# Kernel tuning notes

Hardware: AMD Instinct MI355X
Metric: run time of the kernel (lower is better)

Reference implementation:

```python
import jax, jax.numpy as jnp
import numpy as np

EPS = 1e-5

def _layer_norm(x, w, b):
    mu = jnp.mean(x, axis=-1, keepdims=True)
    var = jnp.mean(jnp.square(x - mu), axis=-1, keepdims=True)
    return (x - mu) * jax.lax.rsqrt(var + EPS) * w + b

def setup_inputs() -> dict:
    key = jax.random.key(0)
    ks = jax.random.split(key, 8)
    B, S, D = 8, 2048, 1024
    image_features = jax.random.normal(ks[0], (B, S, D), dtype=jnp.float32)
    text_features = jax.random.normal(ks[1], (B, S, D), dtype=jnp.float32)
    ln_w = jnp.ones((D,), dtype=jnp.float32)
    ln_b = jnp.zeros((D,), dtype=jnp.float32)
    lim = 1.0 / np.sqrt(D)
    W_img = jax.random.uniform(ks[2], (D, D), minval=-lim, maxval=lim, dtype=jnp.float32)
    b_img = jax.random.uniform(ks[3], (D,), minval=-lim, maxval=lim, dtype=jnp.float32)
    W_txt = jax.random.uniform(ks[4], (D, D), minval=-lim, maxval=lim, dtype=jnp.float32)
    b_txt = jax.random.uniform(ks[5], (D,), minval=-lim, maxval=lim, dtype=jnp.float32)
    return {"image_features": image_features, "text_features": text_features,
            "ln_w": ln_w, "ln_b": ln_b, "W_img": W_img, "b_img": b_img,
            "W_txt": W_txt, "b_txt": b_txt}

def reference(image_features, text_features, ln_w, ln_b, W_img, b_img, W_txt, b_txt):
    D = image_features.shape[-1]
    scale = D ** (-0.5)
    image_norm = _layer_norm(image_features, ln_w, ln_b)
    text_norm = _layer_norm(text_features, ln_w, ln_b)
    # torch Linear: x @ W^T + b
    image_proj = jnp.einsum('bsd,ed->bse', image_norm, W_img) + b_img  # [B,Si,D]
    text_proj = jnp.einsum('btd,ed->bte', text_norm, W_txt) + b_txt    # [B,St,D]
    attn = jnp.einsum('bsd,btd->bst', image_proj, text_proj) * scale   # [B,Si,St]
    attn = jax.nn.softmax(attn, axis=-1)
    image_out = jnp.einsum('bst,btd->bsd', attn, text_proj)            # [B,Si,D]
    text_out = jnp.einsum('bst,bsd->btd', attn, image_proj)            # [B,St,D]
    return (image_out, text_out)
```

## Files before the change

kernel.cpp:

```cpp
#include <hip/hip_runtime.h>


#define DEV __device__ __forceinline__

typedef short s16x8 __attribute__((ext_vector_type(8)));
typedef float f32x4 __attribute__((ext_vector_type(4)));

DEV unsigned short f2bf(float f){
  unsigned u = __float_as_uint(f);
  u = (u + 0x7fffu + ((u >> 16) & 1u)) >> 16;
  return (unsigned short)u;
}
DEV float bf2f(unsigned short s){ return __uint_as_float(((unsigned)s) << 16); }

DEV void ldsload16(const void* g, void* l){
  __builtin_amdgcn_global_load_lds((const __attribute__((address_space(1))) void*)g,
                                   (__attribute__((address_space(3))) void*)l, 16, 0, 0);
}

__global__ __launch_bounds__(256) void k_cvt2(const float* __restrict__ sa,
                                              const float* __restrict__ sb,
                                              unsigned short* __restrict__ da,
                                              unsigned short* __restrict__ db, int n4){
  int i = blockIdx.x * 256 + threadIdx.x;
  const float* s; unsigned short* d; int j;
  if (i < n4){ s = sa; d = da; j = i; }
  else       { s = sb; d = db; j = i - n4; if (j >= n4) return; }
  float4 v = ((const float4*)s)[j];
  ushort4 o;
  o.x = f2bf(v.x); o.y = f2bf(v.y); o.z = f2bf(v.z); o.w = f2bf(v.w);
  ((ushort4*)d)[j] = o;
}

__global__ __launch_bounds__(256) void k_ln2(const float* __restrict__ xa,
                                             const float* __restrict__ xb,
                                             const float* __restrict__ w,
                                             const float* __restrict__ b,
                                             unsigned short* __restrict__ ya,
                                             unsigned short* __restrict__ yb){
  int rb = blockIdx.x, tid = threadIdx.x;
  const float* x; unsigned short* y;
  if (rb < 16384){ x = xa; y = ya; } else { x = xb; y = yb; rb -= 16384; }
  float4 v = ((const float4*)(x + (size_t)rb * 1024))[tid];
  float s  = v.x + v.y + v.z + v.w;
  float s2 = v.x*v.x + v.y*v.y + v.z*v.z + v.w*v.w;
  #pragma unroll
  for (int o = 32; o > 0; o >>= 1){ s += __shfl_xor(s, o, 64); s2 += __shfl_xor(s2, o, 64); }
  __shared__ float sh[8];
  int wv = tid >> 6, ln = tid & 63;
  if (!ln){ sh[wv] = s; sh[4 + wv] = s2; }
  __syncthreads();
  s  = sh[0] + sh[1] + sh[2] + sh[3];
  s2 = sh[4] + sh[5] + sh[6] + sh[7];
  float mean = s * (1.f/1024.f);
  float var  = s2 * (1.f/1024.f) - mean * mean;
  float rstd = rsqrtf(var + 1e-5f);
  float4 w4 = ((const float4*)w)[tid];
  float4 b4 = ((const float4*)b)[tid];
  ushort4 o;
  o.x = f2bf((v.x-mean)*rstd*w4.x + b4.x);
  o.y = f2bf((v.y-mean)*rstd*w4.y + b4.y);
  o.z = f2bf((v.z-mean)*rstd*w4.z + b4.z);
  o.w = f2bf((v.w-mean)*rstd*w4.w + b4.w);
  ((ushort4*)(y + (size_t)rb * 1024))[tid] = o;
}

#define STG(MAT, BASE, LD, T, H) do{                                              \
  ldsload16((BASE) + (size_t)(wave*16 + sfr) * (LD) + (T)*64 + (H)*32 + sq*8,     \
            &MAT[(T)&1][H][wave][0]);                                             \
  ldsload16((BASE) + (size_t)(wave*16 + 128 + sfr) * (LD) + (T)*64 + (H)*32 + sq*8,\
            &MAT[(T)&1][H][wave + 8][0]);                                         \
}while(0)

template<int OUT_BF16, int WRITE_T>
__global__ __launch_bounds__(512, 2) void k_gemm256(const unsigned short* __restrict__ A,
                                                    const unsigned short* __restrict__ Bt,
                                                    void* __restrict__ C,
                                                    unsigned short* __restrict__ ct,
                                                    const float* __restrict__ bias,
                                                    const unsigned short* __restrict__ A2,
                                                    const unsigned short* __restrict__ Bt2,
                                                    void* __restrict__ C2,
                                                    unsigned short* __restrict__ ct2,
                                                    const float* __restrict__ bias2,
                                                    float scale,
                                                    int K, int lda, int ldb, int ldc,
                                                    long sA, long sB, long sC,
                                                    int NBX, int NBY, int NBZ1){
  __shared__ __align__(16) unsigned short SH[65536];
  typedef unsigned short (*Buf)[2][16][512];
  Buf As = (Buf)SH;
  Buf Bs = (Buf)(SH + 32768);
  int nwg = gridDim.x;
  int bid = blockIdx.x;
  int swz = (bid & 7) * (nwg >> 3) + (bid >> 3);
  int bx = swz % NBX; int rem = swz / NBX;
  int by = rem % NBY; int bz = rem / NBY;

  const unsigned short* Ap = A; const unsigned short* Bp = Bt;
  void* Cp = C; unsigned short* ctp = ct; const float* bp = bias;
  if (bz >= NBZ1){ bz -= NBZ1; Ap = A2; Bp = Bt2; Cp = C2; ctp = ct2; bp = bias2; }

  int tid = threadIdx.x, lane = tid & 63, wave = tid >> 6;
  int wm = wave >> 2, wn = wave & 3;
  int q = lane >> 4, fr = lane & 15;
  const unsigned short* Ab = Ap + (size_t)bz * sA + (size_t)by * 256 * lda;
  const unsigned short* Bb = Bp + (size_t)bz * sB + (size_t)bx * 256 * ldb;
  int v   = (lane & 7) ^ ((lane >> 3) & 7);
  int sfr = 2 * (lane >> 3) + (v >> 2);
  int sq  = v & 3;
  int roff = ((fr >> 1) << 6) + (((q + ((fr & 1) << 2)) ^ ((fr >> 1) & 7)) << 3);
  int NT = K >> 6;

  f32x4 acc[8][4];
  #pragma unroll
  for (int m = 0; m < 8; ++m)
    #pragma unroll
    for (int n = 0; n < 4; ++n) acc[m][n] = f32x4{0.f, 0.f, 0.f, 0.f};

  STG(As, Ab, lda, 0, 0); STG(Bs, Bb, ldb, 0, 0);
  STG(As, Ab, lda, 0, 1); STG(Bs, Bb, ldb, 0, 1);
  STG(As, Ab, lda, 1, 0); STG(Bs, Bb, ldb, 1, 0);
  asm volatile("s_waitcnt vmcnt(8)");
  __builtin_amdgcn_s_barrier();

  for (int t = 0; t < NT; ++t){
    const int buf = t & 1;
    s16x8 bfr[4];
    #pragma unroll
    for (int ph = 0; ph < 4; ++ph){
      const int kk = ph >> 1;
      const unsigned short* Ah = &As[buf][kk][0][0];
      const unsigned short* Bh = &Bs[buf][kk][0][0];
      s16x8 af[4];
      if ((ph & 1) == 0){
        #pragma unroll
        for (int n = 0; n < 4; ++n)  bfr[n] = *(const s16x8*)&Bh[(wn*4 + n)*512 + roff];
        #pragma unroll
        for (int mi = 0; mi < 4; ++mi) af[mi] = *(const s16x8*)&Ah[(wm*8 + mi)*512 + roff];
      } else {
        #pragma unroll
        for (int mi = 0; mi < 4; ++mi) af[mi] = *(const s16x8*)&Ah[(wm*8 + 4 + mi)*512 + roff];
      }
      if (ph == 0){ if (t + 1 < NT) STG(As, Ab, lda, t + 1, 1); }
      if (ph == 1){ if (t + 1 < NT) STG(Bs, Bb, ldb, t + 1, 1); }
      if (ph == 2){ if (t + 2 < NT) STG(As, Ab, lda, t + 2, 0); }
      if (ph == 3){ if (t + 2 < NT) STG(Bs, Bb, ldb, t + 2, 0); }
      __builtin_amdgcn_s_barrier();
      asm volatile("s_waitcnt lgkmcnt(0)");
      __builtin_amdgcn_s_setprio(1);
      #pragma unroll
      for (int mi = 0; mi < 4; ++mi)
        #pragma unroll
        for (int n = 0; n < 4; ++n)
          acc[(ph&1)*4 + mi][n] = __builtin_amdgcn_mfma_f32_16x16x32_bf16(
              af[mi], bfr[n], acc[(ph&1)*4 + mi][n], 0, 0, 0);
      __builtin_amdgcn_s_setprio(0);
      if (ph & 1){
        if (t + 2 < NT) asm volatile("s_waitcnt vmcnt(8)");
        else            asm volatile("s_waitcnt vmcnt(0)");
      }
      __builtin_amdgcn_s_barrier();
    }
  }
  size_t cb = (size_t)bz * sC;
  int row0 = by*256 + wm*128 + q*4;
  int col0 = bx*256 + wn*64 + fr;
  #pragma unroll
  for (int m = 0; m < 8; ++m){
    #pragma unroll
    for (int n = 0; n < 4; ++n){
      int col = col0 + n*16;
      float bv = bp ? bp[col] : 0.f;
      #pragma unroll
      for (int j = 0; j < 4; ++j){
        int row = row0 + m*16 + j;
        float vv = acc[m][n][j] * scale + bv;
        if (OUT_BF16) ((unsigned short*)Cp)[cb + (size_t)row*ldc + col] = f2bf(vv);
        else          ((float*)Cp)[cb + (size_t)row*ldc + col] = vv;
      }
    }
  }
  if (WRITE_T){
    unsigned short* LT = SH;
    __syncthreads();
    #pragma unroll
    for (int m = 0; m < 8; ++m){
      #pragma unroll
      for (int n = 0; n < 4; ++n){
        int tr = wn*64 + n*16 + fr;
        int tc = wm*128 + m*16 + q*4;
        float bv = bp ? bp[bx*256 + tr] : 0.f;
        ushort4 pk;
        pk.x = f2bf(acc[m][n][0] * scale + bv);
        pk.y = f2bf(acc[m][n][1] * scale + bv);
        pk.z = f2bf(acc[m][n][2] * scale + bv);
        pk.w = f2bf(acc[m][n][3] * scale + bv);
        int idx = tr*256 + (((tc >> 3) ^ (tr & 7)) << 3) + (tc & 7);
        *(ushort4*)&LT[idx] = pk;
      }
    }
    __syncthreads();
    int bb = by >> 3;
    int r2b = (by & 7) * 256;
    unsigned short* ctb = ctp + (size_t)bb * 2097152 + r2b;
    #pragma unroll
    for (int p = 0; p < 16; ++p){
      int rr = p*16 + wave*2 + (lane >> 5);
      int ci = lane & 31;
      s16x8 rd = *(const s16x8*)&LT[rr*256 + ((ci ^ (rr & 7)) << 3)];
      *(s16x8*)&ctb[(size_t)(bx*256 + rr) * 2048 + ci*8] = rd;
    }
  }
}

__global__ __launch_bounds__(256) void k_transpose(const unsigned short* __restrict__ src,
                                                   unsigned short* __restrict__ dst,
                                                   int R, int C, long sS, long sD){
  __shared__ __align__(16) unsigned short tile[64 * 64];
  int tid = threadIdx.x;
  const unsigned short* sb = src + (size_t)blockIdx.z * sS;
  unsigned short* db = dst + (size_t)blockIdx.z * sD;
  int r0 = blockIdx.y * 64, c0 = blockIdx.x * 64;
  #pragma unroll
  for (int i = 0; i < 2; ++i){
    int ci = i * 256 + tid;
    int row = ci >> 3, cch = ci & 7;
    int pos = cch ^ (row & 7) ^ (row >> 3);
    uint4 v = *(const uint4*)&sb[(size_t)(r0 + row) * C + c0 + cch * 8];
    *(uint4*)&tile[row * 64 + pos * 8] = v;
  }
  __syncthreads();
  int ocp = tid >> 3, og = tid & 7;
  int oc = ocp * 2;
  union { uint4 v; unsigned short us[8]; } o0, o1;
  #pragma unroll
  for (int k = 0; k < 8; ++k){
    int r = og * 8 + k;
    int pos = (oc >> 3) ^ (r & 7) ^ (r >> 3);
    unsigned pr = *(const unsigned*)&tile[r * 64 + pos * 8 + (oc & 7)];
    o0.us[k] = (unsigned short)(pr & 0xffffu);
    o1.us[k] = (unsigned short)(pr >> 16);
  }
  *(uint4*)&db[(size_t)(c0 + oc    ) * R + r0 + og * 8] = o0.v;
  *(uint4*)&db[(size_t)(c0 + oc + 1) * R + r0 + og * 8] = o1.v;
}

__global__ __launch_bounds__(256) void k_softmax(unsigned short* __restrict__ a){
  size_t row = blockIdx.x;
  unsigned short* p = a + row * 2048;
  int tid = threadIdx.x;
  union { uint4 v; unsigned short us[8]; } in, out;
  in.v = *(const uint4*)&p[tid * 8];
  float x[8];
  #pragma unroll
  for (int j = 0; j < 8; ++j) x[j] = bf2f(in.us[j]);
  float mx = x[0];
  #pragma unroll
  for (int j = 1; j < 8; ++j) mx = fmaxf(mx, x[j]);
  #pragma unroll
  for (int o = 32; o > 0; o >>= 1) mx = fmaxf(mx, __shfl_xor(mx, o, 64));
  __shared__ float sh[8];
  int wv = tid >> 6, ln = tid & 63;
  if (!ln) sh[wv] = mx;
  __syncthreads();
  mx = fmaxf(fmaxf(sh[0], sh[1]), fmaxf(sh[2], sh[3]));
  float sm = 0.f, e[8];
  #pragma unroll
  for (int j = 0; j < 8; ++j){ e[j] = __expf(x[j] - mx); sm += e[j]; }
  #pragma unroll
  for (int o = 32; o > 0; o >>= 1) sm += __shfl_xor(sm, o, 64);
  if (!ln) sh[4 + wv] = sm;
  __syncthreads();
  sm = sh[4] + sh[5] + sh[6] + sh[7];
  float inv = 1.f / sm;
  #pragma unroll
  for (int j = 0; j < 8; ++j) out.us[j] = f2bf(e[j] * inv);
  *(uint4*)&p[tid * 8] = out.v;
}

extern "C" void kernel_launch(void* const* d_in, const int* in_sizes, int n_in,
                              void* d_out, int out_size, void* d_ws, size_t ws_size,
                              hipStream_t stream) {
  const float* img  = (const float*)d_in[0];
  const float* txt  = (const float*)d_in[1];
  const float* lnw  = (const float*)d_in[2];
  const float* lnb  = (const float*)d_in[3];
  const float* Wimg = (const float*)d_in[4];
  const float* bimg = (const float*)d_in[5];
  const float* Wtxt = (const float*)d_in[6];
  const float* btxt = (const float*)d_in[7];
  float* out = (float*)d_out;

  char* ws = (char*)d_ws;
  unsigned short* R1 = (unsigned short*)ws;
  unsigned short* R2 = (unsigned short*)(ws + 67108864);
  unsigned short* WB = (unsigned short*)(ws + 134217728);
  unsigned short* R4 = (unsigned short*)(ws + 138412032);

  const long PB = 2097152;
  const long AB = 4194304;

  k_cvt2<<<2048, 256, 0, stream>>>(Wimg, Wtxt, WB, WB + 1048576, 262144);
  k_ln2<<<32768, 256, 0, stream>>>(img, txt, lnw, lnb, R1, R1 + 16777216);
  k_gemm256<1,1><<<512, 512, 0, stream>>>(
      R1,            WB,           R2,            R4,            bimg,
      R1 + 16777216, WB + 1048576, R2 + 16777216, R4 + 16777216, btxt,
      1.f, 1024, 1024, 1024, 1024, 0, 0, 0, 4, 64, 1);
  k_gemm256<1,0><<<512, 512, 0, stream>>>(
      R2, R2 + 16777216, R1, nullptr, nullptr,
      R2, R2 + 16777216, R1, nullptr, nullptr,
      0.03125f, 1024, 1024, 1024, 2048, PB, PB, AB, 8, 8, 8);
  k_softmax<<<16384, 256, 0, stream>>>(R1);
  dim3 gat(32, 32, 8);
  k_transpose<<<gat, 256, 0, stream>>>(R1, R2, 2048, 2048, AB, AB);
  k_gemm256<0,0><<<512, 512, 0, stream>>>(
      R1, R4 + 16777216, out,            nullptr, nullptr,
      R2, R4,            out + 16777216, nullptr, nullptr,
      1.f, 2048, 2048, 2048, 1024, AB, PB, PB, 4, 8, 8);
}
```

Measured before the change: 399.5 us.

## Shrink GEMM tiles to 256x128 with 4 waves and triple-buffered K=32 pipeline

```diff
diff --git a/kernel.cpp b/kernel.cpp
--- a/kernel.cpp
+++ b/kernel.cpp
@@ -65,32 +65,39 @@
   ((ushort4*)(y + (size_t)rb * 1024))[tid] = o;
 }
 
-#define STG(MAT, BASE, LD, T, H) do{                                              \
-  ldsload16((BASE) + (size_t)(wave*16 + sfr) * (LD) + (T)*64 + (H)*32 + sq*8,     \
-            &MAT[(T)&1][H][wave][0]);                                             \
-  ldsload16((BASE) + (size_t)(wave*16 + 128 + sfr) * (LD) + (T)*64 + (H)*32 + sq*8,\
-            &MAT[(T)&1][H][wave + 8][0]);                                         \
+#define STGA(T, SL) do{                                                           \
+  _Pragma("unroll")                                                               \
+  for (int i_ = 0; i_ < 4; ++i_)                                                  \
+    ldsload16(Ab + (size_t)((wave + 4*i_)*16 + sfr) * lda + (T)*32 + sq*8,        \
+              &As[SL][wave + 4*i_][0]);                                           \
 }while(0)
+#define STGB(T, SL) do{                                                           \
+  _Pragma("unroll")                                                               \
+  for (int i_ = 0; i_ < 2; ++i_)                                                  \
+    ldsload16(Bb + (size_t)((wave + 4*i_)*16 + sfr) * ldb + (T)*32 + sq*8,        \
+              &Bs[SL][wave + 4*i_][0]);                                           \
+}while(0)
 
 template<int OUT_BF16, int WRITE_T>
-__global__ __launch_bounds__(512, 2) void k_gemm256(const unsigned short* __restrict__ A,
-                                                    const unsigned short* __restrict__ Bt,
-                                                    void* __restrict__ C,
-                                                    unsigned short* __restrict__ ct,
-                                                    const float* __restrict__ bias,
-                                                    const unsigned short* __restrict__ A2,
-                                                    const unsigned short* __restrict__ Bt2,
-                                                    void* __restrict__ C2,
-                                                    unsigned short* __restrict__ ct2,
-                                                    const float* __restrict__ bias2,
-                                                    float scale,
-                                                    int K, int lda, int ldb, int ldc,
-                                                    long sA, long sB, long sC,
-                                                    int NBX, int NBY, int NBZ1){
-  __shared__ __align__(16) unsigned short SH[65536];
-  typedef unsigned short (*Buf)[2][16][512];
-  Buf As = (Buf)SH;
-  Buf Bs = (Buf)(SH + 32768);
+__global__ __launch_bounds__(256, 2) void k_gemm(const unsigned short* __restrict__ A,
+                                                 const unsigned short* __restrict__ Bt,
+                                                 void* __restrict__ C,
+                                                 unsigned short* __restrict__ ct,
+                                                 const float* __restrict__ bias,
+                                                 const unsigned short* __restrict__ A2,
+                                                 const unsigned short* __restrict__ Bt2,
+                                                 void* __restrict__ C2,
+                                                 unsigned short* __restrict__ ct2,
+                                                 const float* __restrict__ bias2,
+                                                 float scale,
+                                                 int K, int lda, int ldb, int ldc,
+                                                 long sA, long sB, long sC,
+                                                 int NBX, int NBY, int NBZ1){
+  __shared__ __align__(16) unsigned short SH[36864];
+  typedef unsigned short (*BufA)[16][512];
+  typedef unsigned short (*BufB)[8][512];
+  BufA As = (BufA)SH;
+  BufB Bs = (BufB)(SH + 24576);
   int nwg = gridDim.x;
   int bid = blockIdx.x;
   int swz = (bid & 7) * (nwg >> 3) + (bid >> 3);
@@ -102,15 +109,15 @@
   if (bz >= NBZ1){ bz -= NBZ1; Ap = A2; Bp = Bt2; Cp = C2; ctp = ct2; bp = bias2; }
 
   int tid = threadIdx.x, lane = tid & 63, wave = tid >> 6;
-  int wm = wave >> 2, wn = wave & 3;
+  int wm = wave >> 1, wn = wave & 1;
   int q = lane >> 4, fr = lane & 15;
   const unsigned short* Ab = Ap + (size_t)bz * sA + (size_t)by * 256 * lda;
-  const unsigned short* Bb = Bp + (size_t)bz * sB + (size_t)bx * 256 * ldb;
+  const unsigned short* Bb = Bp + (size_t)bz * sB + (size_t)bx * 128 * ldb;
   int v   = (lane & 7) ^ ((lane >> 3) & 7);
   int sfr = 2 * (lane >> 3) + (v >> 2);
   int sq  = v & 3;
   int roff = ((fr >> 1) << 6) + (((q + ((fr & 1) << 2)) ^ ((fr >> 1) & 7)) << 3);
-  int NT = K >> 6;
+  int NT = K >> 5;
 
   f32x4 acc[8][4];
   #pragma unroll
@@ -118,54 +125,50 @@
     #pragma unroll
     for (int n = 0; n < 4; ++n) acc[m][n] = f32x4{0.f, 0.f, 0.f, 0.f};
 
-  STG(As, Ab, lda, 0, 0); STG(Bs, Bb, ldb, 0, 0);
-  STG(As, Ab, lda, 0, 1); STG(Bs, Bb, ldb, 0, 1);
-  STG(As, Ab, lda, 1, 0); STG(Bs, Bb, ldb, 1, 0);
-  asm volatile("s_waitcnt vmcnt(8)");
+  STGA(0, 0); STGB(0, 0);
+  STGA(1, 1); STGB(1, 1);
+  asm volatile("s_waitcnt vmcnt(6)");
   __builtin_amdgcn_s_barrier();
 
+  int rs = 0, ss = 2;
   for (int t = 0; t < NT; ++t){
-    const int buf = t & 1;
-    s16x8 bfr[4];
-    #pragma unroll
-    for (int ph = 0; ph < 4; ++ph){
-      const int kk = ph >> 1;
-      const unsigned short* Ah = &As[buf][kk][0][0];
-      const unsigned short* Bh = &Bs[buf][kk][0][0];
-      s16x8 af[4];
-      if ((ph & 1) == 0){
-        #pragma unroll
-        for (int n = 0; n < 4; ++n)  bfr[n] = *(const s16x8*)&Bh[(wn*4 + n)*512 + roff];
-        #pragma unroll
-        for (int mi = 0; mi < 4; ++mi) af[mi] = *(const s16x8*)&Ah[(wm*8 + mi)*512 + roff];
-      } else {
-        #pragma unroll
-        for (int mi = 0; mi < 4; ++mi) af[mi] = *(const s16x8*)&Ah[(wm*8 + 4 + mi)*512 + roff];
-      }
-      if (ph == 0){ if (t + 1 < NT) STG(As, Ab, lda, t + 1, 1); }
-      if (ph == 1){ if (t + 1 < NT) STG(Bs, Bb, ldb, t + 1, 1); }
-      if (ph == 2){ if (t + 2 < NT) STG(As, Ab, lda, t + 2, 0); }
-      if (ph == 3){ if (t + 2 < NT) STG(Bs, Bb, ldb, t + 2, 0); }
-      __builtin_amdgcn_s_barrier();
-      asm volatile("s_waitcnt lgkmcnt(0)");
-      __builtin_amdgcn_s_setprio(1);
+    s16x8 bfr[4], af[4];
+    #pragma unroll
+    for (int n = 0; n < 4; ++n)  bfr[n] = *(const s16x8*)&Bs[rs][wn*4 + n][roff];
+    #pragma unroll
+    for (int mi = 0; mi < 4; ++mi) af[mi] = *(const s16x8*)&As[rs][wm*8 + mi][roff];
+    if (t + 2 < NT) STGA(t + 2, ss);
+    __builtin_amdgcn_s_barrier();
+    asm volatile("s_waitcnt lgkmcnt(0)");
+    __builtin_amdgcn_s_setprio(1);
+    #pragma unroll
+    for (int mi = 0; mi < 4; ++mi)
       #pragma unroll
-      for (int mi = 0; mi < 4; ++mi)
-        #pragma unroll
-        for (int n = 0; n < 4; ++n)
-          acc[(ph&1)*4 + mi][n] = __builtin_amdgcn_mfma_f32_16x16x32_bf16(
-              af[mi], bfr[n], acc[(ph&1)*4 + mi][n], 0, 0, 0);
-      __builtin_amdgcn_s_setprio(0);
-      if (ph & 1){
-        if (t + 2 < NT) asm volatile("s_waitcnt vmcnt(8)");
-        else            asm volatile("s_waitcnt vmcnt(0)");
-      }
-      __builtin_amdgcn_s_barrier();
-    }
+      for (int n = 0; n < 4; ++n)
+        acc[mi][n] = __builtin_amdgcn_mfma_f32_16x16x32_bf16(af[mi], bfr[n], acc[mi][n], 0, 0, 0);
+    __builtin_amdgcn_s_setprio(0);
+    __builtin_amdgcn_s_barrier();
+    #pragma unroll
+    for (int mi = 0; mi < 4; ++mi) af[mi] = *(const s16x8*)&As[rs][wm*8 + 4 + mi][roff];
+    if (t + 2 < NT) STGB(t + 2, ss);
+    __builtin_amdgcn_s_barrier();
+    asm volatile("s_waitcnt lgkmcnt(0)");
+    __builtin_amdgcn_s_setprio(1);
+    #pragma unroll
+    for (int mi = 0; mi < 4; ++mi)
+      #pragma unroll
+      for (int n = 0; n < 4; ++n)
+        acc[4 + mi][n] = __builtin_amdgcn_mfma_f32_16x16x32_bf16(af[mi], bfr[n], acc[4 + mi][n], 0, 0, 0);
+    __builtin_amdgcn_s_setprio(0);
+    if (t + 2 < NT) asm volatile("s_waitcnt vmcnt(6)");
+    else            asm volatile("s_waitcnt vmcnt(0)");
+    __builtin_amdgcn_s_barrier();
+    rs = (rs == 2) ? 0 : rs + 1;
+    ss = (ss == 2) ? 0 : ss + 1;
   }
   size_t cb = (size_t)bz * sC;
   int row0 = by*256 + wm*128 + q*4;
-  int col0 = bx*256 + wn*64 + fr;
+  int col0 = bx*128 + wn*64 + fr;
   #pragma unroll
   for (int m = 0; m < 8; ++m){
     #pragma unroll
@@ -190,7 +193,7 @@
       for (int n = 0; n < 4; ++n){
         int tr = wn*64 + n*16 + fr;
         int tc = wm*128 + m*16 + q*4;
-        float bv = bp ? bp[bx*256 + tr] : 0.f;
+        float bv = bp ? bp[bx*128 + tr] : 0.f;
         ushort4 pk;
         pk.x = f2bf(acc[m][n][0] * scale + bv);
         pk.y = f2bf(acc[m][n][1] * scale + bv);
@@ -206,10 +209,10 @@
     unsigned short* ctb = ctp + (size_t)bb * 2097152 + r2b;
     #pragma unroll
     for (int p = 0; p < 16; ++p){
-      int rr = p*16 + wave*2 + (lane >> 5);
-      int ci = lane & 31;
+      int rr = p*8 + (tid >> 5);
+      int ci = tid & 31;
       s16x8 rd = *(const s16x8*)&LT[rr*256 + ((ci ^ (rr & 7)) << 3)];
-      *(s16x8*)&ctb[(size_t)(bx*256 + rr) * 2048 + ci*8] = rd;
+      *(s16x8*)&ctb[(size_t)(bx*128 + rr) * 2048 + ci*8] = rd;
     }
   }
 }
@@ -303,19 +306,19 @@
 
   k_cvt2<<<2048, 256, 0, stream>>>(Wimg, Wtxt, WB, WB + 1048576, 262144);
   k_ln2<<<32768, 256, 0, stream>>>(img, txt, lnw, lnb, R1, R1 + 16777216);
-  k_gemm256<1,1><<<512, 512, 0, stream>>>(
+  k_gemm<1,1><<<1024, 256, 0, stream>>>(
       R1,            WB,           R2,            R4,            bimg,
       R1 + 16777216, WB + 1048576, R2 + 16777216, R4 + 16777216, btxt,
-      1.f, 1024, 1024, 1024, 1024, 0, 0, 0, 4, 64, 1);
-  k_gemm256<1,0><<<512, 512, 0, stream>>>(
+      1.f, 1024, 1024, 1024, 1024, 0, 0, 0, 8, 64, 1);
+  k_gemm<1,0><<<1024, 256, 0, stream>>>(
       R2, R2 + 16777216, R1, nullptr, nullptr,
       R2, R2 + 16777216, R1, nullptr, nullptr,
-      0.03125f, 1024, 1024, 1024, 2048, PB, PB, AB, 8, 8, 8);
+      0.03125f, 1024, 1024, 1024, 2048, PB, PB, AB, 16, 8, 8);
   k_softmax<<<16384, 256, 0, stream>>>(R1);
   dim3 gat(32, 32, 8);
   k_transpose<<<gat, 256, 0, stream>>>(R1, R2, 2048, 2048, AB, AB);
-  k_gemm256<0,0><<<512, 512, 0, stream>>>(
+  k_gemm<0,0><<<1024, 256, 0, stream>>>(
       R1, R4 + 16777216, out,            nullptr, nullptr,
       R2, R4,            out + 16777216, nullptr, nullptr,
-      1.f, 2048, 2048, 2048, 1024, AB, PB, PB, 4, 8, 8);
-}
+      1.f, 2048, 2048, 2048, 1024, AB, PB, PB, 8, 8, 8);
+}
```

Result: no change. 407.1 us (+1.9%).
